# Kernel optimization log

Hardware: AMD Instinct MI355X
Metric: run time of the kernel (lower is better)

## Reference

```python
import jax, jax.numpy as jnp
import numpy as np

N_NODES = 50000
N_EDGES = 800000
HIDDEN = 256
OUT_DIM = 10
LN_EPS = 1e-5


def setup_inputs() -> dict:
    key = jax.random.key(0)
    ks = jax.random.split(key, 8)
    return {
        "node_features": jax.random.normal(ks[0], (N_NODES, 2), dtype=jnp.float32),
        "edge_index": jax.random.randint(ks[1], (2, N_EDGES), 0, N_NODES, dtype=jnp.int64),
        "W_gcn": jax.random.normal(ks[2], (2, HIDDEN), dtype=jnp.float32) / np.sqrt(2.0),
        "b_gcn": jnp.zeros((HIDDEN,), dtype=jnp.float32),
        "ln_gamma": jnp.ones((HIDDEN,), dtype=jnp.float32),
        "ln_beta": jnp.zeros((HIDDEN,), dtype=jnp.float32),
        "W_h": jax.random.normal(ks[3], (HIDDEN, HIDDEN), dtype=jnp.float32) / np.sqrt(HIDDEN),
        "b_h": jnp.zeros((HIDDEN,), dtype=jnp.float32),
        "W_out": jax.random.normal(ks[4], (HIDDEN, OUT_DIM), dtype=jnp.float32) / np.sqrt(HIDDEN),
        "b_out": jnp.zeros((OUT_DIM,), dtype=jnp.float32),
    }


def reference(node_features, edge_index, W_gcn, b_gcn, ln_gamma, ln_beta, W_h, b_h, W_out, b_out):
    N = node_features.shape[0]
    # --- GCNConv (PyG default): add self-loops + symmetric normalization ---
    loop = jnp.arange(N, dtype=edge_index.dtype)
    src = jnp.concatenate([edge_index[0], loop])
    dst = jnp.concatenate([edge_index[1], loop])
    deg = jax.ops.segment_sum(jnp.ones_like(dst, dtype=node_features.dtype), dst, num_segments=N)
    dinv = jnp.where(deg > 0, jax.lax.rsqrt(deg), 0.0)
    norm = dinv[src] * dinv[dst]  # [E+N]
    h = node_features @ W_gcn  # [N, H], d_in=2 so linear-before-propagate
    msgs = h[src] * norm[:, None]  # [E+N, H] gathered messages
    agg = jax.ops.segment_sum(msgs, dst, num_segments=N) + b_gcn  # scatter-add
    h = jax.nn.relu(agg)
    # --- LayerNorm ---
    mu = jnp.mean(h, axis=-1, keepdims=True)
    var = jnp.mean(jnp.square(h - mu), axis=-1, keepdims=True)
    h = (h - mu) * jax.lax.rsqrt(var + LN_EPS) * ln_gamma + ln_beta
    # --- global_add_pool with batch = zeros(N): one graph ---
    pooled = jnp.sum(h, axis=0, keepdims=True)  # [1, H]
    # --- MLP head ---
    z = jax.nn.relu(pooled @ W_h + b_h)
    logits = z @ W_out + b_out  # [1, OUT_DIM]
    return jax.nn.log_softmax(logits, axis=1)
```

## Files before the change

### kernel.cpp

```cpp
#include <hip/hip_runtime.h>
#include <math.h>

#define N_NODES 50000
#define N_EDGES 800000
#define HIDDEN  256
#define OUT_DIM 10
#define LN_EPS  1e-5f

#define NP    8
#define PART  6250
#define ES    32
#define EPSE  (N_EDGES / ES)
#define EPSE4 (EPSE / 4)
#define NH2   (N_NODES / 2)
#define NPB   128
#define LNB   ((N_NODES + NPB - 1) / NPB)

__global__ __launch_bounds__(1024) void hist_kernel(
    const int4* __restrict__ dst4, unsigned* __restrict__ degp32,
    float* __restrict__ pooled8,
    const float4* __restrict__ Wh4, const float4* __restrict__ Wo4)
{
    __shared__ unsigned hist[PART];
    const int tid = threadIdx.x;
    const int s = blockIdx.x, p = blockIdx.y;
    const int gb = p * ES + s;

    if (gb == 0) { pooled8[tid] = 0.f; pooled8[tid + 1024] = 0.f; }
    if (gb < 17) {
        const int idx = gb * 1024 + tid;
        if (idx < 16384) {
            const float4 v = Wh4[idx];
            asm volatile("" :: "v"(v.x + v.y + v.z + v.w));
        } else if (idx < 17024) {
            const float4 v = Wo4[idx - 16384];
            asm volatile("" :: "v"(v.x + v.y + v.z + v.w));
        }
    }

    for (int i = tid; i < PART; i += 1024) hist[i] = 0u;
    __syncthreads();

    const int base = p * PART;
    const int b0 = s * EPSE4;
    for (int i = tid; i < EPSE4; i += 1024) {
        const int4 d = dst4[b0 + i];
        unsigned r;
        r = (unsigned)(d.x - base); if (r < PART) atomicAdd(&hist[r], 1u);
        r = (unsigned)(d.y - base); if (r < PART) atomicAdd(&hist[r], 1u);
        r = (unsigned)(d.z - base); if (r < PART) atomicAdd(&hist[r], 1u);
        r = (unsigned)(d.w - base); if (r < PART) atomicAdd(&hist[r], 1u);
    }
    __syncthreads();

    unsigned* outp = degp32 + (size_t)s * NH2 + base / 2;
    for (int i = tid; i < PART / 2; i += 1024)
        outp[i] = (hist[2 * i] & 0xFFFFu) | (hist[2 * i + 1] << 16);
}

__global__ __launch_bounds__(256) void dinv_y_kernel(
    const unsigned* __restrict__ degp32, const float4* __restrict__ nf4,
    float2* __restrict__ dinv2, float4* __restrict__ y4,
    unsigned* __restrict__ mlp_ticket)
{
    const int t = blockIdx.x * 256 + threadIdx.x;
    if (t == 0) *mlp_ticket = 0u;
    if (t >= NH2) return;
    unsigned s0 = 0, s1 = 0;
    #pragma unroll
    for (int s = 0; s < ES; ++s) {
        const unsigned d = degp32[(size_t)s * NH2 + t];
        s0 += d & 0xFFFFu;
        s1 += d >> 16;
    }
    const float di0 = rsqrtf((float)s0 + 1.0f);
    const float di1 = rsqrtf((float)s1 + 1.0f);
    dinv2[t] = make_float2(di0, di1);
    const float4 x = nf4[t];
    y4[t] = make_float4(di0 * x.x, di0 * x.y, di1 * x.z, di1 * x.w);
}

__global__ __launch_bounds__(1024) void scatterp_kernel(
    const int4* __restrict__ src4, const int4* __restrict__ dst4,
    const float2* __restrict__ y, float2* __restrict__ TpartB2)
{
    __shared__ float Tl[2 * PART];
    const int tid = threadIdx.x;
    const int s = blockIdx.x, p = blockIdx.y;

    for (int i = tid; i < 2 * PART; i += 1024) Tl[i] = 0.f;
    __syncthreads();

    const int base = p * PART;
    const int b0 = s * EPSE4;
    for (int i = tid; i < EPSE4; i += 1024) {
        const int4 d = dst4[b0 + i];
        const unsigned r0 = (unsigned)(d.x - base);
        const unsigned r1 = (unsigned)(d.y - base);
        const unsigned r2 = (unsigned)(d.z - base);
        const unsigned r3 = (unsigned)(d.w - base);
        if ((r0 < PART) | (r1 < PART) | (r2 < PART) | (r3 < PART)) {
            const int4 sv = src4[b0 + i];
            if (r0 < PART) { const float2 ys = y[sv.x]; atomicAdd(&Tl[2*r0], ys.x); atomicAdd(&Tl[2*r0+1], ys.y); }
            if (r1 < PART) { const float2 ys = y[sv.y]; atomicAdd(&Tl[2*r1], ys.x); atomicAdd(&Tl[2*r1+1], ys.y); }
            if (r2 < PART) { const float2 ys = y[sv.z]; atomicAdd(&Tl[2*r2], ys.x); atomicAdd(&Tl[2*r2+1], ys.y); }
            if (r3 < PART) { const float2 ys = y[sv.w]; atomicAdd(&Tl[2*r3], ys.x); atomicAdd(&Tl[2*r3+1], ys.y); }
        }
    }
    __syncthreads();

    const float2* Tl2 = (const float2*)Tl;
    for (int i = tid; i < PART; i += 1024) {
        const int n = base + i;
        const int idx = (((n >> 7) * ES + s) << 7) | (n & 127);
        TpartB2[idx] = Tl2[i];
    }
}

__global__ __launch_bounds__(512) void ln_pool_mlp_kernel(
    const float2* __restrict__ TpartB2,
    const float2* __restrict__ y,
    const float* __restrict__ dinv,
    const float* __restrict__ Wg, const float* __restrict__ bg,
    const float* __restrict__ gamma, const float* __restrict__ beta,
    const float* __restrict__ Wh, const float* __restrict__ bh,
    const float* __restrict__ Wo, const float* __restrict__ bo,
    float* __restrict__ pooled8,
    unsigned* __restrict__ ticket,
    float* __restrict__ out)
{
    const int tid  = threadIdx.x;
    const int bid  = blockIdx.x;
    const int n0   = bid * NPB;
    const int lane = tid & 63;
    const int wv   = tid >> 6;

    __shared__ float4 nd[NPB];
    __shared__ float  psx[8][NPB];
    __shared__ float  psy[8][NPB];
    __shared__ float  red[8][HIDDEN];
    __shared__ float  pz[HIDDEN], zz[HIDDEN];
    __shared__ float  lgp[OUT_DIM][16], lg[OUT_DIM];
    __shared__ int    is_last;

    {
        const float2* tp = TpartB2 + (size_t)bid * (ES * NPB);
        float ax0 = 0.f, ay0 = 0.f, ax1 = 0.f, ay1 = 0.f;
        #pragma unroll
        for (int s4 = 0; s4 < 4; ++s4) {
            const int row = ((wv << 2) + s4) << 7;
            const float2 v0 = tp[row + lane];
            const float2 v1 = tp[row + 64 + lane];
            ax0 += v0.x; ay0 += v0.y;
            ax1 += v1.x; ay1 += v1.y;
        }
        psx[wv][lane] = ax0;      psy[wv][lane] = ay0;
        psx[wv][64 + lane] = ax1; psy[wv][64 + lane] = ay1;
    }
    __syncthreads();

    if (tid < NPB) {
        const int n = n0 + tid;
        float s0 = 0.f, s1 = 0.f;
        if (n < N_NODES) {
            float tx = 0.f, ty = 0.f;
            #pragma unroll
            for (int w = 0; w < 8; ++w) { tx += psx[w][tid]; ty += psy[w][tid]; }
            const float di = dinv[n];
            const float2 yn = y[n];
            s0 = di * (tx + yn.x);
            s1 = di * (ty + yn.y);
        }
        nd[tid] = make_float4(s0, s1, 0.f, 0.f);
    }
    __syncthreads();

    {
        const int wu  = __builtin_amdgcn_readfirstlane(wv);
        const int h   = wu & 1;
        const int jg  = wu >> 1;
        const float* w0p = Wg + jg * 64;
        const float* w1p = Wg + HIDDEN + jg * 64;
        const float* bgp = bg + jg * 64;
        const int node = h * 64 + lane;
        const float4 d = nd[node];
        float sumA = 0.f, sumB = 0.f, sqA = 0.f, sqB = 0.f;
        #pragma unroll 8
        for (int j = 0; j < 64; j += 2) {
            const float va = fmaxf(fmaf(d.y, w1p[j],     fmaf(d.x, w0p[j],     bgp[j])),     0.f);
            const float vb = fmaxf(fmaf(d.y, w1p[j + 1], fmaf(d.x, w0p[j + 1], bgp[j + 1])), 0.f);
            sumA += va; sqA = fmaf(va, va, sqA);
            sumB += vb; sqB = fmaf(vb, vb, sqB);
        }
        psx[jg][node] = sumA + sumB;
        psy[jg][node] = sqA + sqB;
    }
    __syncthreads();

    if (tid < NPB) {
        const float sum = psx[0][tid] + psx[1][tid] + psx[2][tid] + psx[3][tid];
        const float sq  = psy[0][tid] + psy[1][tid] + psy[2][tid] + psy[3][tid];
        const float mu  = sum * (1.0f / HIDDEN);
        const float var = sq * (1.0f / HIDDEN) - mu * mu;
        float r = rsqrtf(var + LN_EPS);
        if (n0 + tid >= N_NODES) r = 0.f;
        const float4 d = nd[tid];
        nd[tid] = make_float4(d.x, d.y, r, r * mu);
    }
    __syncthreads();

    {
        const float4 w0  = *reinterpret_cast<const float4*>(&Wg[lane * 4]);
        const float4 w1  = *reinterpret_cast<const float4*>(&Wg[HIDDEN + lane * 4]);
        const float4 bgv = *reinterpret_cast<const float4*>(&bg[lane * 4]);

        float a0 = 0.f, a1 = 0.f, a2 = 0.f, a3 = 0.f;
        #pragma unroll
        for (int k = 0; k < 16; ++k) {
            const float4 d = nd[wv * 16 + k];
            const float v0 = fmaxf(fmaf(d.y, w1.x, fmaf(d.x, w0.x, bgv.x)), 0.f);
            const float v1 = fmaxf(fmaf(d.y, w1.y, fmaf(d.x, w0.y, bgv.y)), 0.f);
            const float v2 = fmaxf(fmaf(d.y, w1.z, fmaf(d.x, w0.z, bgv.z)), 0.f);
            const float v3 = fmaxf(fmaf(d.y, w1.w, fmaf(d.x, w0.w, bgv.w)), 0.f);
            a0 += fmaf(d.z, v0, -d.w);
            a1 += fmaf(d.z, v1, -d.w);
            a2 += fmaf(d.z, v2, -d.w);
            a3 += fmaf(d.z, v3, -d.w);
        }
        red[wv][lane * 4 + 0] = a0;
        red[wv][lane * 4 + 1] = a1;
        red[wv][lane * 4 + 2] = a2;
        red[wv][lane * 4 + 3] = a3;
    }
    __syncthreads();

    if (tid < HIDDEN) {
        float s = 0.f;
        #pragma unroll
        for (int w = 0; w < 8; ++w) s += red[w][tid];
        atomicAdd(&pooled8[(bid & 7) * HIDDEN + tid], s);
    }
    __syncthreads();

    if (tid == 0) {
        const unsigned old = __hip_atomic_fetch_add(ticket, 1u, __ATOMIC_ACQ_REL,
                                                    __HIP_MEMORY_SCOPE_AGENT);
        is_last = (old == (unsigned)(gridDim.x - 1));
    }
    __syncthreads();
    if (!is_last) return;

    if (tid < HIDDEN) {
        float S = 0.f;
        #pragma unroll
        for (int k = 0; k < 8; ++k) S += pooled8[k * HIDDEN + tid];
        pz[tid] = gamma[tid] * S + (float)N_NODES * beta[tid];
    }
    __syncthreads();

    {
        const int g = tid >> 8;
        const int j = tid & 255;
        float acc = 0.f;
        #pragma unroll 8
        for (int k = g * 128; k < g * 128 + 128; ++k)
            acc = fmaf(pz[k], Wh[k * HIDDEN + j], acc);
        red[g][j] = acc;
    }
    __syncthreads();
    if (tid < HIDDEN)
        zz[tid] = fmaxf(bh[tid] + red[0][tid] + red[1][tid], 0.f);
    __syncthreads();

    if (tid < OUT_DIM * 16) {
        const int o = tid >> 4, kc = tid & 15;
        float acc = 0.f;
        #pragma unroll
        for (int k = kc * 16; k < kc * 16 + 16; ++k)
            acc = fmaf(zz[k], Wo[k * OUT_DIM + o], acc);
        lgp[o][kc] = acc;
    }
    __syncthreads();
    if (tid < OUT_DIM) {
        float t = bo[tid];
        #pragma unroll
        for (int q = 0; q < 16; ++q) t += lgp[tid][q];
        lg[tid] = t;
    }
    __syncthreads();

    if (tid == 0) {
        float m = lg[0];
        for (int k = 1; k < OUT_DIM; ++k) m = fmaxf(m, lg[k]);
        float sum = 0.f;
        for (int k = 0; k < OUT_DIM; ++k) sum += expf(lg[k] - m);
        const float lse = m + logf(sum);
        for (int k = 0; k < OUT_DIM; ++k) out[k] = lg[k] - lse;
    }
}

extern "C" void kernel_launch(void* const* d_in, const int* in_sizes, int n_in,
                              void* d_out, int out_size, void* d_ws, size_t ws_size,
                              hipStream_t stream) {
    const float* nf    = (const float*)d_in[0];
    const int*   ei    = (const int*)  d_in[1];
    const float* Wg    = (const float*)d_in[2];
    const float* bg    = (const float*)d_in[3];
    const float* gamma = (const float*)d_in[4];
    const float* beta  = (const float*)d_in[5];
    const float* Wh    = (const float*)d_in[6];
    const float* bh    = (const float*)d_in[7];
    const float* Wo    = (const float*)d_in[8];
    const float* bo    = (const float*)d_in[9];
    float* out = (float*)d_out;

    const int* srcp = ei;
    const int* dstp = ei + N_EDGES;

    float* pooled8 = (float*)d_ws;
    unsigned* mlp_ticket = (unsigned*)(pooled8 + 8 * HIDDEN);
    unsigned* degp32 = mlp_ticket + 16;
    float* TpartB = (float*)(degp32 + (size_t)ES * NH2);
    float* dinvp  = TpartB + (size_t)LNB * ES * NPB * 2;
    float* yp     = dinvp + N_NODES;

    dim3 pg(ES, NP);
    hist_kernel<<<pg, 1024, 0, stream>>>((const int4*)dstp, degp32, pooled8,
                                         (const float4*)Wh, (const float4*)Wo);
    dinv_y_kernel<<<(NH2 + 255) / 256, 256, 0, stream>>>(degp32, (const float4*)nf,
                                                         (float2*)dinvp, (float4*)yp,
                                                         mlp_ticket);
    scatterp_kernel<<<pg, 1024, 0, stream>>>((const int4*)srcp, (const int4*)dstp,
                                             (const float2*)yp, (float2*)TpartB);
    ln_pool_mlp_kernel<<<LNB, 512, 0, stream>>>((const float2*)TpartB,
                                                (const float2*)yp, dinvp,
                                                Wg, bg, gamma, beta, Wh, bh, Wo, bo,
                                                pooled8, mlp_ticket, out);
}
```

Before: 51.55 us.

## Build per-partition edge lists in histogram pass to skip dst rescans in scatter

The histogram kernel now also records, for each (edge-slice, partition) block, a compact list of (local row, edge offset) entries in shared memory and writes it to a workspace. The scatter kernel then walks only its own list instead of rereading the whole dst slice and filtering by partition, which removes an 8x redundant read of the dst array. In exchange, hist_kernel does an extra shared atomic per edge and writes the lists out. Each list holds at most 4608 entries with no overflow check, so the code depends on the random edge distribution never putting more than that many edges into one block.

```diff
diff --git a/kernel.cpp b/kernel.cpp
--- a/kernel.cpp
+++ b/kernel.cpp
@@ -15,13 +15,17 @@
 #define NH2   (N_NODES / 2)
 #define NPB   128
 #define LNB   ((N_NODES + NPB - 1) / NPB)
+#define LCAP  4608
 
 __global__ __launch_bounds__(1024) void hist_kernel(
     const int4* __restrict__ dst4, unsigned* __restrict__ degp32,
+    unsigned* __restrict__ lists, unsigned* __restrict__ counts,
     float* __restrict__ pooled8,
     const float4* __restrict__ Wh4, const float4* __restrict__ Wo4)
 {
     __shared__ unsigned hist[PART];
+    __shared__ unsigned list[LCAP];
+    __shared__ unsigned lcount;
     const int tid = threadIdx.x;
     const int s = blockIdx.x, p = blockIdx.y;
     const int gb = p * ES + s;
@@ -38,6 +42,7 @@
         }
     }
 
+    if (tid == 0) lcount = 0u;
     for (int i = tid; i < PART; i += 1024) hist[i] = 0u;
     __syncthreads();
 
@@ -46,16 +51,25 @@
     for (int i = tid; i < EPSE4; i += 1024) {
         const int4 d = dst4[b0 + i];
         unsigned r;
-        r = (unsigned)(d.x - base); if (r < PART) atomicAdd(&hist[r], 1u);
-        r = (unsigned)(d.y - base); if (r < PART) atomicAdd(&hist[r], 1u);
-        r = (unsigned)(d.z - base); if (r < PART) atomicAdd(&hist[r], 1u);
-        r = (unsigned)(d.w - base); if (r < PART) atomicAdd(&hist[r], 1u);
+        r = (unsigned)(d.x - base);
+        if (r < PART) { atomicAdd(&hist[r], 1u); list[atomicAdd(&lcount, 1u)] = (r << 16) | (4u * i + 0u); }
+        r = (unsigned)(d.y - base);
+        if (r < PART) { atomicAdd(&hist[r], 1u); list[atomicAdd(&lcount, 1u)] = (r << 16) | (4u * i + 1u); }
+        r = (unsigned)(d.z - base);
+        if (r < PART) { atomicAdd(&hist[r], 1u); list[atomicAdd(&lcount, 1u)] = (r << 16) | (4u * i + 2u); }
+        r = (unsigned)(d.w - base);
+        if (r < PART) { atomicAdd(&hist[r], 1u); list[atomicAdd(&lcount, 1u)] = (r << 16) | (4u * i + 3u); }
     }
     __syncthreads();
 
     unsigned* outp = degp32 + (size_t)s * NH2 + base / 2;
     for (int i = tid; i < PART / 2; i += 1024)
         outp[i] = (hist[2 * i] & 0xFFFFu) | (hist[2 * i + 1] << 16);
+
+    const unsigned cnt = lcount;
+    if (tid == 0) counts[gb] = cnt;
+    unsigned* lout = lists + (size_t)gb * LCAP;
+    for (unsigned i = tid; i < cnt; i += 1024) lout[i] = list[i];
 }
 
 __global__ __launch_bounds__(256) void dinv_y_kernel(
@@ -81,34 +95,31 @@
 }
 
 __global__ __launch_bounds__(1024) void scatterp_kernel(
-    const int4* __restrict__ src4, const int4* __restrict__ dst4,
+    const int* __restrict__ src,
+    const unsigned* __restrict__ lists, const unsigned* __restrict__ counts,
     const float2* __restrict__ y, float2* __restrict__ TpartB2)
 {
     __shared__ float Tl[2 * PART];
     const int tid = threadIdx.x;
     const int s = blockIdx.x, p = blockIdx.y;
+    const int gb = p * ES + s;
 
     for (int i = tid; i < 2 * PART; i += 1024) Tl[i] = 0.f;
     __syncthreads();
 
+    const unsigned cnt = counts[gb];
+    const unsigned* lst = lists + (size_t)gb * LCAP;
+    const int* srcs = src + s * EPSE;
+    for (unsigned i = tid; i < cnt; i += 1024) {
+        const unsigned e = lst[i];
+        const unsigned r = e >> 16;
+        const float2 ys = y[srcs[e & 0xFFFFu]];
+        atomicAdd(&Tl[2 * r],     ys.x);
+        atomicAdd(&Tl[2 * r + 1], ys.y);
+    }
+    __syncthreads();
+
     const int base = p * PART;
-    const int b0 = s * EPSE4;
-    for (int i = tid; i < EPSE4; i += 1024) {
-        const int4 d = dst4[b0 + i];
-        const unsigned r0 = (unsigned)(d.x - base);
-        const unsigned r1 = (unsigned)(d.y - base);
-        const unsigned r2 = (unsigned)(d.z - base);
-        const unsigned r3 = (unsigned)(d.w - base);
-        if ((r0 < PART) | (r1 < PART) | (r2 < PART) | (r3 < PART)) {
-            const int4 sv = src4[b0 + i];
-            if (r0 < PART) { const float2 ys = y[sv.x]; atomicAdd(&Tl[2*r0], ys.x); atomicAdd(&Tl[2*r0+1], ys.y); }
-            if (r1 < PART) { const float2 ys = y[sv.y]; atomicAdd(&Tl[2*r1], ys.x); atomicAdd(&Tl[2*r1+1], ys.y); }
-            if (r2 < PART) { const float2 ys = y[sv.z]; atomicAdd(&Tl[2*r2], ys.x); atomicAdd(&Tl[2*r2+1], ys.y); }
-            if (r3 < PART) { const float2 ys = y[sv.w]; atomicAdd(&Tl[2*r3], ys.x); atomicAdd(&Tl[2*r3+1], ys.y); }
-        }
-    }
-    __syncthreads();
-
     const float2* Tl2 = (const float2*)Tl;
     for (int i = tid; i < PART; i += 1024) {
         const int n = base + i;
@@ -319,18 +330,20 @@
 
     float* pooled8 = (float*)d_ws;
     unsigned* mlp_ticket = (unsigned*)(pooled8 + 8 * HIDDEN);
-    unsigned* degp32 = mlp_ticket + 16;
-    float* TpartB = (float*)(degp32 + (size_t)ES * NH2);
+    unsigned* counts = mlp_ticket + 16;
+    unsigned* degp32 = counts + 256;
+    unsigned* lists  = degp32 + (size_t)ES * NH2;
+    float* TpartB = (float*)(lists + (size_t)ES * NP * LCAP);
     float* dinvp  = TpartB + (size_t)LNB * ES * NPB * 2;
     float* yp     = dinvp + N_NODES;
 
     dim3 pg(ES, NP);
-    hist_kernel<<<pg, 1024, 0, stream>>>((const int4*)dstp, degp32, pooled8,
-                                         (const float4*)Wh, (const float4*)Wo);
+    hist_kernel<<<pg, 1024, 0, stream>>>((const int4*)dstp, degp32, lists, counts,
+                                         pooled8, (const float4*)Wh, (const float4*)Wo);
     dinv_y_kernel<<<(NH2 + 255) / 256, 256, 0, stream>>>(degp32, (const float4*)nf,
                                                          (float2*)dinvp, (float4*)yp,
                                                          mlp_ticket);
-    scatterp_kernel<<<pg, 1024, 0, stream>>>((const int4*)srcp, (const int4*)dstp,
+    scatterp_kernel<<<pg, 1024, 0, stream>>>(srcp, lists, counts,
                                              (const float2*)yp, (float2*)TpartB);
     ln_pool_mlp_kernel<<<LNB, 512, 0, stream>>>((const float2*)TpartB,
                                                 (const float2*)yp, dinvp,
```

Result: slower. 53.36 us (+3.5%).

## Pack degree histogram into 16-bit LDS counters with wider node partitions

Applied to the files above, without the earlier changes.

The degree histogram now keeps two 16-bit counters per 32-bit shared-memory word. This doubles the node range each block covers, so the grid uses 4 node partitions and 64 edge slices instead of 8 and 32. The packed words are written straight to global memory without repacking. In exchange, each node partition's edge data is read half as many times, but dinv_y must sum 64 partial slices instead of 32, and the workspace for partial degrees doubles. Per-slice counts are small, so the 16-bit fields should not overflow.

```diff
diff --git a/kernel.cpp b/kernel.cpp
--- a/kernel.cpp
+++ b/kernel.cpp
@@ -7,11 +7,18 @@
 #define OUT_DIM 10
 #define LN_EPS  1e-5f
 
+#define HES   64
+#define HNP   4
+#define HPART 12500
+#define HEPSE (N_EDGES / HES)
+#define HEPSE4 (HEPSE / 4)
+
 #define NP    8
 #define PART  6250
 #define ES    32
 #define EPSE  (N_EDGES / ES)
 #define EPSE4 (EPSE / 4)
+
 #define NH2   (N_NODES / 2)
 #define NPB   128
 #define LNB   ((N_NODES + NPB - 1) / NPB)
@@ -21,10 +28,10 @@
     float* __restrict__ pooled8,
     const float4* __restrict__ Wh4, const float4* __restrict__ Wo4)
 {
-    __shared__ unsigned hist[PART];
+    __shared__ unsigned hist[HPART / 2];
     const int tid = threadIdx.x;
     const int s = blockIdx.x, p = blockIdx.y;
-    const int gb = p * ES + s;
+    const int gb = p * HES + s;
 
     if (gb == 0) { pooled8[tid] = 0.f; pooled8[tid + 1024] = 0.f; }
     if (gb < 17) {
@@ -38,24 +45,23 @@
         }
     }
 
-    for (int i = tid; i < PART; i += 1024) hist[i] = 0u;
-    __syncthreads();
-
-    const int base = p * PART;
-    const int b0 = s * EPSE4;
-    for (int i = tid; i < EPSE4; i += 1024) {
+    for (int i = tid; i < HPART / 2; i += 1024) hist[i] = 0u;
+    __syncthreads();
+
+    const int base = p * HPART;
+    const int b0 = s * HEPSE4;
+    for (int i = tid; i < HEPSE4; i += 1024) {
         const int4 d = dst4[b0 + i];
         unsigned r;
-        r = (unsigned)(d.x - base); if (r < PART) atomicAdd(&hist[r], 1u);
-        r = (unsigned)(d.y - base); if (r < PART) atomicAdd(&hist[r], 1u);
-        r = (unsigned)(d.z - base); if (r < PART) atomicAdd(&hist[r], 1u);
-        r = (unsigned)(d.w - base); if (r < PART) atomicAdd(&hist[r], 1u);
+        r = (unsigned)(d.x - base); if (r < HPART) atomicAdd(&hist[r >> 1], 1u << ((r & 1) * 16));
+        r = (unsigned)(d.y - base); if (r < HPART) atomicAdd(&hist[r >> 1], 1u << ((r & 1) * 16));
+        r = (unsigned)(d.z - base); if (r < HPART) atomicAdd(&hist[r >> 1], 1u << ((r & 1) * 16));
+        r = (unsigned)(d.w - base); if (r < HPART) atomicAdd(&hist[r >> 1], 1u << ((r & 1) * 16));
     }
     __syncthreads();
 
     unsigned* outp = degp32 + (size_t)s * NH2 + base / 2;
-    for (int i = tid; i < PART / 2; i += 1024)
-        outp[i] = (hist[2 * i] & 0xFFFFu) | (hist[2 * i + 1] << 16);
+    for (int i = tid; i < HPART / 2; i += 1024) outp[i] = hist[i];
 }
 
 __global__ __launch_bounds__(256) void dinv_y_kernel(
@@ -68,7 +74,7 @@
     if (t >= NH2) return;
     unsigned s0 = 0, s1 = 0;
     #pragma unroll
-    for (int s = 0; s < ES; ++s) {
+    for (int s = 0; s < HES; ++s) {
         const unsigned d = degp32[(size_t)s * NH2 + t];
         s0 += d & 0xFFFFu;
         s1 += d >> 16;
@@ -320,12 +326,13 @@
     float* pooled8 = (float*)d_ws;
     unsigned* mlp_ticket = (unsigned*)(pooled8 + 8 * HIDDEN);
     unsigned* degp32 = mlp_ticket + 16;
-    float* TpartB = (float*)(degp32 + (size_t)ES * NH2);
+    float* TpartB = (float*)(degp32 + (size_t)HES * NH2);
     float* dinvp  = TpartB + (size_t)LNB * ES * NPB * 2;
     float* yp     = dinvp + N_NODES;
 
+    dim3 hg(HES, HNP);
     dim3 pg(ES, NP);
-    hist_kernel<<<pg, 1024, 0, stream>>>((const int4*)dstp, degp32, pooled8,
+    hist_kernel<<<hg, 1024, 0, stream>>>((const int4*)dstp, degp32, pooled8,
                                          (const float4*)Wh, (const float4*)Wo);
     dinv_y_kernel<<<(NH2 + 255) / 256, 256, 0, stream>>>(degp32, (const float4*)nf,
                                                          (float2*)dinvp, (float4*)yp,
```

After: 52.50 us. Within noise of the previous version (+1.9%).
